# Performance work log

Measured on AMD Instinct MI355X. Metric: run time of the kernel, lower is better.

## Reference

```python
import jax, jax.numpy as jnp
import numpy as np

N = 100000
D = 128      # embedding_dim
HID = 32     # hidden per head
HEADS = 4
OUT_C = 64
E = 1600000
NEG_SLOPE = 0.2


def setup_inputs() -> dict:
    key = jax.random.key(0)
    ks = jax.random.split(key, 12)
    inp = {}
    inp["x_indices"] = jnp.arange(N, dtype=jnp.int64)
    inp["ei"] = jax.random.randint(ks[0], (2, E), 0, N, dtype=jnp.int64)
    # parameters
    inp["emb"] = jax.random.normal(ks[1], (N, D), dtype=jnp.float32)
    # conv1: in=D, out=HID per head, HEADS heads, concat
    s1 = 1.0 / np.sqrt(D)
    inp["W1"] = jax.random.normal(ks[2], (D, HEADS * HID), dtype=jnp.float32) * s1
    inp["a_src1"] = jax.random.normal(ks[3], (HEADS, HID), dtype=jnp.float32) * s1
    inp["a_dst1"] = jax.random.normal(ks[4], (HEADS, HID), dtype=jnp.float32) * s1
    inp["b1"] = jnp.zeros((HEADS * HID,), dtype=jnp.float32)
    # conv2: in=HEADS*HID, out=OUT_C, 1 head
    s2 = 1.0 / np.sqrt(HEADS * HID)
    inp["W2"] = jax.random.normal(ks[5], (HEADS * HID, OUT_C), dtype=jnp.float32) * s2
    inp["a_src2"] = jax.random.normal(ks[6], (1, OUT_C), dtype=jnp.float32) * s2
    inp["a_dst2"] = jax.random.normal(ks[7], (1, OUT_C), dtype=jnp.float32) * s2
    inp["b2"] = jnp.zeros((OUT_C,), dtype=jnp.float32)
    return inp


def gat_conv(x, src, dst, W, a_src, a_dst, b, heads, out_ch, concat):
    # x: [N, Din]; src/dst: [E'] (self-loops already included)
    n = x.shape[0]
    h = (x @ W).reshape(n, heads, out_ch)          # [N, H, C]
    alpha_s = jnp.sum(h * a_src, axis=-1)          # [N, H]
    alpha_d = jnp.sum(h * a_dst, axis=-1)          # [N, H]
    e = alpha_s[src] + alpha_d[dst]                # [E', H]
    e = jnp.where(e > 0, e, NEG_SLOPE * e)         # leaky_relu
    # segment softmax over incoming edges per destination node
    m = jax.ops.segment_max(e, dst, num_segments=n)      # [N, H]
    ex = jnp.exp(e - m[dst])
    den = jax.ops.segment_sum(ex, dst, num_segments=n)   # [N, H]
    a = ex / den[dst]                              # [E', H]  (self-loops guarantee den>0)
    msg = h[src] * a[:, :, None]                   # [E', H, C]
    out = jax.ops.segment_sum(msg, dst, num_segments=n)  # [N, H, C]
    if concat:
        out = out.reshape(n, heads * out_ch)
    else:
        out = out.mean(axis=1)
    return out + b


def reference(x_indices, ei, emb, W1, a_src1, a_dst1, b1, W2, a_src2, a_dst2, b2):
    n = emb.shape[0]
    # PyG GATConv default add_self_loops=True
    loop = jnp.arange(n, dtype=ei.dtype)
    src = jnp.concatenate([ei[0], loop])
    dst = jnp.concatenate([ei[1], loop])
    x = emb[x_indices]                                  # embedding lookup
    x = jax.nn.elu(gat_conv(x, src, dst, W1, a_src1, a_dst1, b1, HEADS, HID, True))
    # dropout p=0.5 is identity in eval mode
    return gat_conv(x, src, dst, W2, a_src2, a_dst2, b2, 1, OUT_C, True)
```

## Files before the change

kernel.cpp:

```cpp
#include <hip/hip_runtime.h>
#include <math.h>

#define NEG_SLOPE 0.2f
#define BK_SHIFT 8

typedef __attribute__((ext_vector_type(2))) float v2f;
typedef __attribute__((ext_vector_type(8))) short bf16x8;
typedef __attribute__((ext_vector_type(4))) float f32x4;

__device__ __forceinline__ float leaky(float x) { return x > 0.f ? x : NEG_SLOPE * x; }
__device__ __forceinline__ float dot4(float4 a, float4 b) {
    return a.x * b.x + a.y * b.y + a.z * b.z + a.w * b.w;
}
__device__ __forceinline__ unsigned short f2bf(float f) {
    unsigned int x = __float_as_uint(f);
    unsigned int r = (x + 0x7fffu + ((x >> 16) & 1u)) >> 16;
    return (unsigned short)r;
}
__device__ __forceinline__ float bflo(unsigned int u) { return __uint_as_float(u << 16); }
__device__ __forceinline__ float bfhi(unsigned int u) { return __uint_as_float(u & 0xffff0000u); }


__global__ void __launch_bounds__(256) bcount_kernel(const int* __restrict__ ei, int E, int E2,
                                                     int K, int* __restrict__ bcounts) {
    __shared__ int h[512];
    int t = threadIdx.x;
    h[t] = 0; h[t + 256] = 0;
    __syncthreads();
    int base = blockIdx.x * 4096;
#pragma unroll 4
    for (int i = 0; i < 16; i++) {
        int e = base + i * 256 + t;
        if (e < E2) {
            int dst = (e < E) ? ei[E + e] : (e - E);
            atomicAdd(&h[dst >> BK_SHIFT], 1);
        }
    }
    __syncthreads();
    for (int b = t; b < K; b += 256) {
        int c = h[b];
        if (c) atomicAdd(&bcounts[b], c);
    }
}

__global__ void __launch_bounds__(512) bscan_kernel(const int* __restrict__ bcounts, int K,
                                                    int* __restrict__ bbase, int* __restrict__ bcursor) {
    __shared__ int s[512];
    int t = threadIdx.x;
    int v = (t < K) ? bcounts[t] : 0;
    s[t] = v;
    __syncthreads();
    for (int off = 1; off < 512; off <<= 1) {
        int u = (t >= off) ? s[t - off] : 0;
        __syncthreads();
        s[t] += u;
        __syncthreads();
    }
    if (t < K) {
        int ex = s[t] - v;
        bbase[t] = ex;
        bcursor[t] = ex;
    }
    if (t == 511) bbase[K] = s[511];
}

__global__ void __launch_bounds__(256) bscatter_kernel(const int* __restrict__ ei, int E, int E2,
                                                       int K, int* __restrict__ bcursor,
                                                       unsigned int* __restrict__ bedges) {
    __shared__ int hist[512], pre[512], lcur[512], gbase[512], psum[256];
    __shared__ unsigned int stage[4096];
    __shared__ unsigned short binof[4096];
    int t = threadIdx.x;
    hist[t] = 0; hist[t + 256] = 0;
    __syncthreads();
    int base = blockIdx.x * 4096;
    int cnt = min(4096, E2 - base);
    int s_[16], d_[16];
#pragma unroll
    for (int i = 0; i < 16; i++) {
        int e = base + i * 256 + t;
        if (e < E2) {
            int ss, dd;
            if (e < E) { ss = ei[e]; dd = ei[E + e]; }
            else       { ss = e - E; dd = ss; }
            s_[i] = ss; d_[i] = dd;
            atomicAdd(&hist[dd >> BK_SHIFT], 1);
        }
    }
    __syncthreads();
    int a0 = hist[2 * t], a1 = hist[2 * t + 1];
    psum[t] = a0 + a1;
    __syncthreads();
    for (int off = 1; off < 256; off <<= 1) {
        int u = (t >= off) ? psum[t - off] : 0;
        __syncthreads();
        psum[t] += u;
        __syncthreads();
    }
    int pex = psum[t] - (a0 + a1);
    pre[2 * t] = pex;
    pre[2 * t + 1] = pex + a0;
    __syncthreads();
    for (int b = t; b < K; b += 256) {
        int c = hist[b];
        if (c) gbase[b] = atomicAdd(&bcursor[b], c);
    }
    lcur[t] = pre[t]; lcur[t + 256] = pre[t + 256];
    __syncthreads();
#pragma unroll
    for (int i = 0; i < 16; i++) {
        int e = base + i * 256 + t;
        if (e < E2) {
            int bin = d_[i] >> BK_SHIFT;
            int p = atomicAdd(&lcur[bin], 1);
            stage[p] = ((unsigned)s_[i] << 8) | (unsigned)(d_[i] & 255);
            binof[p] = (unsigned short)bin;
        }
    }
    __syncthreads();
    for (int i = t; i < cnt; i += 256) {
        unsigned int ed = stage[i];
        int bin = (int)binof[i];
        bedges[gbase[bin] + (i - pre[bin])] = ed;
    }
}

__global__ void __launch_bounds__(256) bcsr_kernel(const unsigned int* __restrict__ bedges,
                                                   const int* __restrict__ bbase, int N,
                                                   int* __restrict__ counts, int* __restrict__ indptr,
                                                   int* __restrict__ csr) {
    __shared__ int hist[256], scn[256], cur[256];
    int b = blockIdx.x;
    int t = threadIdx.x;
    int base = bbase[b];
    int cnt = bbase[b + 1] - base;
    hist[t] = 0;
    __syncthreads();
    for (int i = t; i < cnt; i += 256) {
        atomicAdd(&hist[bedges[base + i] & 255u], 1);
    }
    __syncthreads();
    int v = hist[t];
    scn[t] = v;
    __syncthreads();
    for (int off = 1; off < 256; off <<= 1) {
        int u = (t >= off) ? scn[t - off] : 0;
        __syncthreads();
        scn[t] += u;
        __syncthreads();
    }
    int ex = scn[t] - v;
    int d = (b << BK_SHIFT) + t;
    if (d < N) { counts[d] = v; indptr[d] = base + ex; }
    cur[t] = ex;
    __syncthreads();
    for (int i = t; i < cnt; i += 256) {
        unsigned int ed = bedges[base + i];
        int p = atomicAdd(&cur[ed & 255u], 1);
        csr[base + p] = (int)(ed >> 8);
    }
}


__global__ void w2pack_kernel(const float* __restrict__ W2, unsigned short* __restrict__ w2p) {
    int i = blockIdx.x * 256 + threadIdx.x;
    if (i < 8192) {
        int t = i >> 11;
        int c = (i >> 9) & 3;
        int l = (i >> 3) & 63;
        int j = i & 7;
        int k = t * 32 + (l >> 4) * 8 + j;
        int col = c * 16 + (l & 15);
        w2p[i] = f2bf(W2[k * 64 + col]);
    }
}


__device__ __forceinline__ void fma16(float4 xv, float4 wv0, float4 wv1,
                                      float4 wv2, float4 wv3, float4& a) {
    a.x = fmaf(xv.x, wv0.x, a.x); a.y = fmaf(xv.x, wv0.y, a.y);
    a.z = fmaf(xv.x, wv0.z, a.z); a.w = fmaf(xv.x, wv0.w, a.w);
    a.x = fmaf(xv.y, wv1.x, a.x); a.y = fmaf(xv.y, wv1.y, a.y);
    a.z = fmaf(xv.y, wv1.z, a.z); a.w = fmaf(xv.y, wv1.w, a.w);
    a.x = fmaf(xv.z, wv2.x, a.x); a.y = fmaf(xv.z, wv2.y, a.y);
    a.z = fmaf(xv.z, wv2.z, a.z); a.w = fmaf(xv.z, wv2.w, a.w);
    a.x = fmaf(xv.w, wv3.x, a.x); a.y = fmaf(xv.w, wv3.y, a.y);
    a.z = fmaf(xv.w, wv3.z, a.z); a.w = fmaf(xv.w, wv3.w, a.w);
}


__global__ __launch_bounds__(256) void gemm1_kernel(const float* __restrict__ emb,
                             const int* __restrict__ xidx,
                             const float* __restrict__ W1,
                             unsigned short* __restrict__ h1b,
                             const float* __restrict__ a_s1, const float* __restrict__ a_d1,
                             float* __restrict__ as1, float* __restrict__ ad1, int N) {
    __shared__ float xs[64][64];
    __shared__ float ws[64][128];
    int tid = threadIdx.x;
    int r0 = blockIdx.x * 64;
    int tr = tid >> 5;
    int tc = tid & 31;
    float4 acc[8];
#pragma unroll
    for (int i = 0; i < 8; i++) acc[i] = make_float4(0.f, 0.f, 0.f, 0.f);
    const float4* W4 = (const float4*)W1;
    const float4* emb4 = (const float4*)emb;
    float4* ws4 = (float4*)ws;
    float4* xs4 = (float4*)xs;

    for (int half = 0; half < 2; half++) {
        float4 wbuf[8];
#pragma unroll
        for (int j = 0; j < 8; j++) wbuf[j] = W4[half * 2048 + tid + j * 256];
        float4 xbuf[4];
#pragma unroll
        for (int j = 0; j < 4; j++) {
            int idx = tid + j * 256;
            int r = idx >> 4, c = idx & 15;
            int row = r0 + r;
            float4 v = make_float4(0.f, 0.f, 0.f, 0.f);
            if (row < N) {
                int s = xidx[row];
                v = emb4[(size_t)s * 32 + half * 16 + c];
            }
            xbuf[j] = v;
        }
        __syncthreads();
#pragma unroll
        for (int j = 0; j < 8; j++) ws4[tid + j * 256] = wbuf[j];
#pragma unroll
        for (int j = 0; j < 4; j++) xs4[tid + j * 256] = xbuf[j];
        __syncthreads();
        for (int k = 0; k < 64; k += 4) {
            float4 wv0 = *(const float4*)&ws[k][tc * 4];
            float4 wv1 = *(const float4*)&ws[k + 1][tc * 4];
            float4 wv2 = *(const float4*)&ws[k + 2][tc * 4];
            float4 wv3 = *(const float4*)&ws[k + 3][tc * 4];
#pragma unroll
            for (int i = 0; i < 8; i++) {
                float4 xv = *(const float4*)&xs[tr * 8 + i][k];
                fma16(xv, wv0, wv1, wv2, wv3, acc[i]);
            }
        }
    }
    int colbase = tc * 4;
    int h = tc >> 3;
    int off = (tc & 7) * 4;
    float4 av = *(const float4*)&a_s1[h * 32 + off];
    float4 dv = *(const float4*)&a_d1[h * 32 + off];
#pragma unroll
    for (int i = 0; i < 8; i++) {
        int row = r0 + tr * 8 + i;
        if (row < N) {
            ushort4 pk;
            pk.x = f2bf(acc[i].x); pk.y = f2bf(acc[i].y);
            pk.z = f2bf(acc[i].z); pk.w = f2bf(acc[i].w);
            *(ushort4*)&h1b[(size_t)row * 128 + colbase] = pk;
        }
        float ps = dot4(acc[i], av);
        float pd = dot4(acc[i], dv);
        ps += __shfl_xor(ps, 1); pd += __shfl_xor(pd, 1);
        ps += __shfl_xor(ps, 2); pd += __shfl_xor(pd, 2);
        ps += __shfl_xor(ps, 4); pd += __shfl_xor(pd, 4);
        if ((tc & 7) == 0 && row < N) {
            as1[row * 4 + h] = ps;
            ad1[row * 4 + h] = pd;
        }
    }
}


__device__ __forceinline__ void edge_fma(uint4 u0, float w, v2f* acc) {
    v2f wv = {w, w};
    v2f t;
    t.x = bflo(u0.x); t.y = bfhi(u0.x); acc[0] += wv * t;
    t.x = bflo(u0.y); t.y = bfhi(u0.y); acc[1] += wv * t;
    t.x = bflo(u0.z); t.y = bfhi(u0.z); acc[2] += wv * t;
    t.x = bflo(u0.w); t.y = bfhi(u0.w); acc[3] += wv * t;
}

__device__ __forceinline__ void accum_tbl1(int srcReg, const float* __restrict__ ew, int mcount,
                                           const uint4* __restrict__ h1v4,
                                           int lanebase, int sub, int cg, int hh, v2f* acc) {
    int b = 0;
    for (; b + 8 <= mcount; b += 8) {
        int i0 = b + sub, i1 = b + 2 + sub, i2 = b + 4 + sub, i3 = b + 6 + sub;
        int s0 = __shfl(srcReg, lanebase + i0);
        int s1 = __shfl(srcReg, lanebase + i1);
        int s2 = __shfl(srcReg, lanebase + i2);
        int s3 = __shfl(srcReg, lanebase + i3);
        float w_0 = ew[i0 * 4 + hh];
        float w_1 = ew[i1 * 4 + hh];
        float w_2 = ew[i2 * 4 + hh];
        float w_3 = ew[i3 * 4 + hh];
        uint4 u0 = h1v4[(unsigned)(s0 * 16 + cg)];
        uint4 u1 = h1v4[(unsigned)(s1 * 16 + cg)];
        uint4 u2 = h1v4[(unsigned)(s2 * 16 + cg)];
        uint4 u3 = h1v4[(unsigned)(s3 * 16 + cg)];
        edge_fma(u0, w_0, acc);
        edge_fma(u1, w_1, acc);
        edge_fma(u2, w_2, acc);
        edge_fma(u3, w_3, acc);
    }
    if (b + 4 <= mcount) {
        int i0 = b + sub, i1 = b + 2 + sub;
        int s0 = __shfl(srcReg, lanebase + i0);
        int s1 = __shfl(srcReg, lanebase + i1);
        float w_0 = ew[i0 * 4 + hh];
        float w_1 = ew[i1 * 4 + hh];
        uint4 u0 = h1v4[(unsigned)(s0 * 16 + cg)];
        uint4 u1 = h1v4[(unsigned)(s1 * 16 + cg)];
        edge_fma(u0, w_0, acc);
        edge_fma(u1, w_1, acc);
        b += 4;
    }
    if (b + 2 <= mcount) {
        int i0 = b + sub;
        int s0 = __shfl(srcReg, lanebase + i0);
        float w_0 = ew[i0 * 4 + hh];
        uint4 u0 = h1v4[(unsigned)(s0 * 16 + cg)];
        edge_fma(u0, w_0, acc);
        b += 2;
    }
    if (b < mcount) {
        int s0 = __shfl(srcReg, lanebase + b);
        if (sub == 0) {
            float w_0 = ew[b * 4 + hh];
            uint4 u0 = h1v4[(unsigned)(s0 * 16 + cg)];
            edge_fma(u0, w_0, acc);
        }
    }
}

__global__ void __launch_bounds__(256)
agg1_kernel(const int* __restrict__ csr, const int* __restrict__ indptr,
            const int* __restrict__ counts, const float* __restrict__ as1,
            const float* __restrict__ ad1, const unsigned short* __restrict__ h1b,
            const float* __restrict__ b1, const unsigned short* __restrict__ w2p,
            const float* __restrict__ a_s2, const float* __restrict__ a_d2,
            unsigned short* __restrict__ h2b, float* __restrict__ as2,
            float* __restrict__ ad2, int N) {
    __shared__ __attribute__((aligned(16))) float ewt[4][2][128];
    __shared__ __attribute__((aligned(16))) unsigned short w2s[8192];
    int tid = threadIdx.x;
    {
        const uint4* w4 = (const uint4*)w2p;
        uint4* s4 = (uint4*)w2s;
        for (int i = tid; i < 1024; i += 256) s4[i] = w4[i];
    }
    __syncthreads();

    int lane = tid & 63;
    int wv = tid >> 6;
    int l32 = lane & 31;
    int lanebase = lane & 32;
    int n = blockIdx.x * 8 + wv * 2 + (lane >> 5);
    bool valid = (n < N);
    int nsafe = valid ? n : 0;
    int start = indptr[nsafe];
    int cnt = valid ? counts[nsafe] : 0;
    float4 ad4 = ((const float4*)ad1)[nsafe];

    int src0 = 0;
    float4 p0 = make_float4(0.f, 0.f, 0.f, 0.f);
    if (l32 < cnt) {
        src0 = csr[start + l32];
        float4 a = ((const float4*)as1)[src0];
        p0.x = __expf(leaky(a.x + ad4.x));
        p0.y = __expf(leaky(a.y + ad4.y));
        p0.z = __expf(leaky(a.z + ad4.z));
        p0.w = __expf(leaky(a.w + ad4.w));
    }
    float4 l4 = p0;
    if (cnt > 32) {
        for (int base = 32; base < cnt; base += 32) {
            if (base + l32 < cnt) {
                int s = csr[start + base + l32];
                float4 a = ((const float4*)as1)[s];
                l4.x += __expf(leaky(a.x + ad4.x));
                l4.y += __expf(leaky(a.y + ad4.y));
                l4.z += __expf(leaky(a.z + ad4.z));
                l4.w += __expf(leaky(a.w + ad4.w));
            }
        }
    }
#pragma unroll
    for (int off = 16; off >= 1; off >>= 1) {
        l4.x += __shfl_xor(l4.x, off);
        l4.y += __shfl_xor(l4.y, off);
        l4.z += __shfl_xor(l4.z, off);
        l4.w += __shfl_xor(l4.w, off);
    }
    float4 li = make_float4(1.f / l4.x, 1.f / l4.y, 1.f / l4.z, 1.f / l4.w);
    float4 w0 = make_float4(p0.x * li.x, p0.y * li.y, p0.z * li.z, p0.w * li.w);

    float* ew = ewt[wv][lane >> 5];
    *(float4*)&ew[l32 * 4] = w0;

    int sub = l32 >> 4;
    int cg = lane & 15;
    int hh = cg >> 2;
    const uint4* h1v4 = (const uint4*)h1b;
    v2f acc[4];
    acc[0] = acc[1] = acc[2] = acc[3] = (v2f){0.f, 0.f};
    accum_tbl1(src0, ew, min(cnt, 32), h1v4, lanebase, sub, cg, hh, acc);
    if (cnt > 32) {
        for (int base = 32; base < cnt; base += 32) {
            int srcc = 0;
            float4 wc = make_float4(0.f, 0.f, 0.f, 0.f);
            if (base + l32 < cnt) {
                srcc = csr[start + base + l32];
                float4 a = ((const float4*)as1)[srcc];
                wc.x = __expf(leaky(a.x + ad4.x)) * li.x;
                wc.y = __expf(leaky(a.y + ad4.y)) * li.y;
                wc.z = __expf(leaky(a.z + ad4.z)) * li.z;
                wc.w = __expf(leaky(a.w + ad4.w)) * li.w;
            }
            *(float4*)&ew[l32 * 4] = wc;
            accum_tbl1(srcc, ew, min(cnt - base, 32), h1v4, lanebase, sub, cg, hh, acc);
        }
    }
#pragma unroll
    for (int i = 0; i < 4; i++) {
        acc[i].x += __shfl_xor(acc[i].x, 16);
        acc[i].y += __shfl_xor(acc[i].y, 16);
    }
    unsigned short* xa = (unsigned short*)&ewt[wv][0][0];
    if (l32 < 16) {
        const float4* b4 = (const float4*)b1;
        float4 ba = b4[cg * 2], bb = b4[cg * 2 + 1];
        float o[8];
        o[0] = acc[0].x + ba.x; o[1] = acc[0].y + ba.y;
        o[2] = acc[1].x + ba.z; o[3] = acc[1].y + ba.w;
        o[4] = acc[2].x + bb.x; o[5] = acc[2].y + bb.y;
        o[6] = acc[3].x + bb.z; o[7] = acc[3].y + bb.w;
#pragma unroll
        for (int j = 0; j < 8; j++) o[j] = (o[j] > 0.f) ? o[j] : (__expf(o[j]) - 1.f);
        uint4 pk;
        pk.x = (unsigned)f2bf(o[0]) | ((unsigned)f2bf(o[1]) << 16);
        pk.y = (unsigned)f2bf(o[2]) | ((unsigned)f2bf(o[3]) << 16);
        pk.z = (unsigned)f2bf(o[4]) | ((unsigned)f2bf(o[5]) << 16);
        pk.w = (unsigned)f2bf(o[6]) | ((unsigned)f2bf(o[7]) << 16);
        *(uint4*)&xa[cg * 16 + (lane >> 5) * 8] = pk;
    }
    int rowA = lane & 15;
    int kb = lane >> 4;
    f32x4 hacc[4];
#pragma unroll
    for (int c = 0; c < 4; c++) hacc[c] = (f32x4){0.f, 0.f, 0.f, 0.f};
#pragma unroll
    for (int t = 0; t < 4; t++) {
        bf16x8 af = {0, 0, 0, 0, 0, 0, 0, 0};
        if (rowA < 2) af = *(const bf16x8*)&xa[(t * 4 + kb) * 16 + rowA * 8];
#pragma unroll
        for (int c = 0; c < 4; c++) {
            bf16x8 bf = *(const bf16x8*)&w2s[((t * 4 + c) * 64 + lane) * 8];
            hacc[c] = __builtin_amdgcn_mfma_f32_16x16x32_bf16(af, bf, hacc[c], 0, 0, 0);
        }
    }
    int na = blockIdx.x * 8 + wv * 2;
    int nb = na + 1;
    bool va = (na < N), vb = (nb < N);
    if (lane < 16) {
        float psa = 0.f, pda = 0.f, psb = 0.f, pdb = 0.f;
#pragma unroll
        for (int c = 0; c < 4; c++) {
            float h0 = hacc[c][0];
            float h1r = hacc[c][1];
            float asv = a_s2[c * 16 + lane];
            float adv = a_d2[c * 16 + lane];
            psa = fmaf(h0, asv, psa); pda = fmaf(h0, adv, pda);
            psb = fmaf(h1r, asv, psb); pdb = fmaf(h1r, adv, pdb);
            if (va) h2b[(size_t)na * 64 + c * 16 + lane] = f2bf(h0);
            if (vb) h2b[(size_t)nb * 64 + c * 16 + lane] = f2bf(h1r);
        }
#pragma unroll
        for (int off = 8; off >= 1; off >>= 1) {
            psa += __shfl_xor(psa, off); pda += __shfl_xor(pda, off);
            psb += __shfl_xor(psb, off); pdb += __shfl_xor(pdb, off);
        }
        if (lane == 0) {
            if (va) { as2[na] = psa; ad2[na] = pda; }
            if (vb) { as2[nb] = psb; ad2[nb] = pdb; }
        }
    }
}


__device__ __forceinline__ void accum2(int srcReg, float wReg, int mcount,
                                       const uint4* __restrict__ h2v4,
                                       int lanebase, int sub, int cg, v2f* acc) {
    int b = 0;
    for (; b + 16 <= mcount; b += 16) {
        int i0 = b + sub, i1 = b + 4 + sub, i2 = b + 8 + sub, i3 = b + 12 + sub;
        int s0 = __shfl(srcReg, lanebase + i0);
        int s1 = __shfl(srcReg, lanebase + i1);
        int s2 = __shfl(srcReg, lanebase + i2);
        int s3 = __shfl(srcReg, lanebase + i3);
        float w_0 = __shfl(wReg, lanebase + i0);
        float w_1 = __shfl(wReg, lanebase + i1);
        float w_2 = __shfl(wReg, lanebase + i2);
        float w_3 = __shfl(wReg, lanebase + i3);
        uint4 u0 = h2v4[(unsigned)(s0 * 8 + cg)];
        uint4 u1 = h2v4[(unsigned)(s1 * 8 + cg)];
        uint4 u2 = h2v4[(unsigned)(s2 * 8 + cg)];
        uint4 u3 = h2v4[(unsigned)(s3 * 8 + cg)];
        edge_fma(u0, w_0, acc);
        edge_fma(u1, w_1, acc);
        edge_fma(u2, w_2, acc);
        edge_fma(u3, w_3, acc);
    }
    if (b + 8 <= mcount) {
        int i0 = b + sub, i1 = b + 4 + sub;
        int s0 = __shfl(srcReg, lanebase + i0);
        int s1 = __shfl(srcReg, lanebase + i1);
        float w_0 = __shfl(wReg, lanebase + i0);
        float w_1 = __shfl(wReg, lanebase + i1);
        uint4 u0 = h2v4[(unsigned)(s0 * 8 + cg)];
        uint4 u1 = h2v4[(unsigned)(s1 * 8 + cg)];
        edge_fma(u0, w_0, acc);
        edge_fma(u1, w_1, acc);
        b += 8;
    }
    if (b + 4 <= mcount) {
        int i0 = b + sub;
        int s0 = __shfl(srcReg, lanebase + i0);
        float w_0 = __shfl(wReg, lanebase + i0);
        uint4 u0 = h2v4[(unsigned)(s0 * 8 + cg)];
        edge_fma(u0, w_0, acc);
        b += 4;
    }
    if (b < mcount) {
        int rem = mcount - b;
        int i0 = b + sub;
        int ic = min(i0, mcount - 1);
        int s0 = __shfl(srcReg, lanebase + ic);
        float w_0 = __shfl(wReg, lanebase + ic);
        if (sub < rem) {
            uint4 u0 = h2v4[(unsigned)(s0 * 8 + cg)];
            edge_fma(u0, w_0, acc);
        }
    }
}

__global__ void __launch_bounds__(256)
agg2_kernel(const int* __restrict__ csr, const int* __restrict__ indptr,
            const int* __restrict__ counts, const float* __restrict__ as2,
            const float* __restrict__ ad2, const unsigned short* __restrict__ h2b,
            const float* __restrict__ b2, float* __restrict__ out, int N) {
    int lane = threadIdx.x & 63;
    int l32 = lane & 31;
    int lanebase = lane & 32;
    int n = blockIdx.x * 8 + (threadIdx.x >> 6) * 2 + (lane >> 5);
    if (n >= N) return;
    int start = indptr[n];
    int cnt = counts[n];
    float ad = ad2[n];

    int src0 = 0;
    float p0 = 0.f;
    if (l32 < cnt) {
        src0 = csr[start + l32];
        p0 = __expf(leaky(as2[src0] + ad));
    }
    float l = p0;
    if (cnt > 32) {
        for (int base = 32; base < cnt; base += 32) {
            if (base + l32 < cnt)
                l += __expf(leaky(as2[csr[start + base + l32]] + ad));
        }
    }
#pragma unroll
    for (int off = 16; off >= 1; off >>= 1) l += __shfl_xor(l, off);
    float li = 1.f / l;
    float w0 = p0 * li;

    int sub = l32 >> 3;
    int cg = lane & 7;
    const uint4* h2v4 = (const uint4*)h2b;
    v2f acc[4];
    acc[0] = acc[1] = acc[2] = acc[3] = (v2f){0.f, 0.f};
    accum2(src0, w0, min(cnt, 32), h2v4, lanebase, sub, cg, acc);
    if (cnt > 32) {
        for (int base = 32; base < cnt; base += 32) {
            int srcc = 0;
            float wc = 0.f;
            if (base + l32 < cnt) {
                srcc = csr[start + base + l32];
                wc = __expf(leaky(as2[srcc] + ad)) * li;
            }
            accum2(srcc, wc, min(cnt - base, 32), h2v4, lanebase, sub, cg, acc);
        }
    }
#pragma unroll
    for (int i = 0; i < 4; i++) {
        acc[i].x += __shfl_xor(acc[i].x, 8);
        acc[i].x += __shfl_xor(acc[i].x, 16);
        acc[i].y += __shfl_xor(acc[i].y, 8);
        acc[i].y += __shfl_xor(acc[i].y, 16);
    }
    if (l32 < 8) {
        const float4* b4 = (const float4*)b2;
        float4 ba = b4[cg * 2], bb = b4[cg * 2 + 1];
        float4 o0, o1;
        o0.x = acc[0].x + ba.x; o0.y = acc[0].y + ba.y;
        o0.z = acc[1].x + ba.z; o0.w = acc[1].y + ba.w;
        o1.x = acc[2].x + bb.x; o1.y = acc[2].y + bb.y;
        o1.z = acc[3].x + bb.z; o1.w = acc[3].y + bb.w;
        float4* orow = (float4*)&out[(size_t)n * 64 + cg * 8];
        orow[0] = o0;
        orow[1] = o1;
    }
}


extern "C" void kernel_launch(void* const* d_in, const int* in_sizes, int n_in,
                              void* d_out, int out_size, void* d_ws, size_t ws_size,
                              hipStream_t stream) {
    const int*   xidx = (const int*)d_in[0];
    const int*   ei   = (const int*)d_in[1];
    const float* emb  = (const float*)d_in[2];
    const float* W1   = (const float*)d_in[3];
    const float* a_s1 = (const float*)d_in[4];
    const float* a_d1 = (const float*)d_in[5];
    const float* b1   = (const float*)d_in[6];
    const float* W2   = (const float*)d_in[7];
    const float* a_s2 = (const float*)d_in[8];
    const float* a_d2 = (const float*)d_in[9];
    const float* b2   = (const float*)d_in[10];
    float* out = (float*)d_out;

    const int N  = in_sizes[0];
    const int E  = in_sizes[1] / 2;
    const int E2 = E + N;
    const int K  = (N + 255) >> BK_SHIFT;

    int* ws_i    = (int*)d_ws;
    int* counts  = ws_i;
    int* indptr  = ws_i + N;
    int* bcounts = ws_i + 2 * (size_t)N;
    int* bbase   = ws_i + 2 * (size_t)N + 512;
    int* bcursor = ws_i + 2 * (size_t)N + 1032;
    int* csr     = ws_i + 2 * (size_t)N + 1544;
    size_t fbase = ((size_t)(2 * (size_t)N + 1544 + E2) + 3) & ~(size_t)3;
    float* ws_f = (float*)d_ws;
    unsigned short* h1b = (unsigned short*)(ws_f + fbase);
    float* region2 = ws_f + fbase + (size_t)N * 64;
    unsigned short* h2b = (unsigned short*)region2;
    float* as2 = region2 + (size_t)N * 32;
    float* ad2 = region2 + (size_t)N * 33;
    unsigned short* w2p = (unsigned short*)(region2 + (size_t)N * 34);
    float* as1 = ws_f + fbase + (size_t)N * 128;
    float* ad1 = as1 + (size_t)N * 4;
    unsigned int* bedges = (unsigned int*)region2;

    int nchunks = (E2 + 4095) / 4096;
    hipMemsetAsync(bcounts, 0, (size_t)K * sizeof(int), stream);
    bcount_kernel<<<nchunks, 256, 0, stream>>>(ei, E, E2, K, bcounts);
    bscan_kernel<<<1, 512, 0, stream>>>(bcounts, K, bbase, bcursor);
    bscatter_kernel<<<nchunks, 256, 0, stream>>>(ei, E, E2, K, bcursor, bedges);
    bcsr_kernel<<<K, 256, 0, stream>>>(bedges, bbase, N, counts, indptr, csr);

    gemm1_kernel<<<(N + 63) / 64, 256, 0, stream>>>(emb, xidx, W1, h1b, a_s1, a_d1, as1, ad1, N);

    w2pack_kernel<<<32, 256, 0, stream>>>(W2, w2p);

    agg1_kernel<<<(N + 7) / 8, 256, 0, stream>>>(csr, indptr, counts, as1, ad1, h1b, b1,
                                                 w2p, a_s2, a_d2, h2b, as2, ad2, N);

    agg2_kernel<<<(N + 7) / 8, 256, 0, stream>>>(csr, indptr, counts, as2, ad2, h2b, b2, out, N);
}
```

Baseline: 401.3 us.

## Move first-layer GEMM to split-bf16 MFMA and merge prep kernels

Replaces the FP32 scalar-FMA tiled GEMM for layer 1 with bf16 MFMA 16x16x32 instructions. A hi/lo split (three MFMAs per tile) keeps accuracy close to FP32. A new prep kernel packs W1 into hi/lo bf16 fragments, packs W2, and zeroes the bucket counters, replacing the memset and the separate w2pack launch. This removes a launch and shifts the GEMM onto matrix cores, but triples the MFMA work and adds bf16 conversion cost per element. The attention-score reduction now uses 16-lane shuffles.

```diff
diff --git a/kernel.cpp b/kernel.cpp
--- a/kernel.cpp
+++ b/kernel.cpp
@@ -9,9 +9,6 @@
 typedef __attribute__((ext_vector_type(4))) float f32x4;
 
 __device__ __forceinline__ float leaky(float x) { return x > 0.f ? x : NEG_SLOPE * x; }
-__device__ __forceinline__ float dot4(float4 a, float4 b) {
-    return a.x * b.x + a.y * b.y + a.z * b.z + a.w * b.w;
-}
 __device__ __forceinline__ unsigned short f2bf(float f) {
     unsigned int x = __float_as_uint(f);
     unsigned int r = (x + 0x7fffu + ((x >> 16) & 1u)) >> 16;
@@ -19,6 +16,33 @@
 }
 __device__ __forceinline__ float bflo(unsigned int u) { return __uint_as_float(u << 16); }
 __device__ __forceinline__ float bfhi(unsigned int u) { return __uint_as_float(u & 0xffff0000u); }
+
+
+__global__ void __launch_bounds__(256) prep_kernel(const float* __restrict__ W1,
+                                                   const float* __restrict__ W2,
+                                                   unsigned short* __restrict__ w1ph,
+                                                   unsigned short* __restrict__ w1pl,
+                                                   unsigned short* __restrict__ w2p,
+                                                   int* __restrict__ bcounts) {
+    int i = blockIdx.x * 256 + threadIdx.x;
+    if (i < 16384) {
+        int j = i & 7, l = (i >> 3) & 63, c = (i >> 9) & 7, t = i >> 12;
+        int k = t * 32 + ((l >> 4) << 3) + j;
+        int col = c * 16 + (l & 15);
+        float v = W1[k * 128 + col];
+        unsigned short hi = f2bf(v);
+        w1ph[i] = hi;
+        w1pl[i] = f2bf(v - __uint_as_float((unsigned)hi << 16));
+    } else if (i < 16384 + 8192) {
+        int i2 = i - 16384;
+        int t = i2 >> 11, c = (i2 >> 9) & 3, l = (i2 >> 3) & 63, j = i2 & 7;
+        int k = t * 32 + (l >> 4) * 8 + j;
+        int col = c * 16 + (l & 15);
+        w2p[i2] = f2bf(W2[k * 64 + col]);
+    } else if (i < 16384 + 8192 + 512) {
+        bcounts[i - 16384 - 8192] = 0;
+    }
+}
 
 
 __global__ void __launch_bounds__(256) bcount_kernel(const int* __restrict__ ei, int E, int E2,
@@ -162,110 +186,103 @@
 }
 
 
-__global__ void w2pack_kernel(const float* __restrict__ W2, unsigned short* __restrict__ w2p) {
-    int i = blockIdx.x * 256 + threadIdx.x;
-    if (i < 8192) {
-        int t = i >> 11;
-        int c = (i >> 9) & 3;
-        int l = (i >> 3) & 63;
-        int j = i & 7;
-        int k = t * 32 + (l >> 4) * 8 + j;
-        int col = c * 16 + (l & 15);
-        w2p[i] = f2bf(W2[k * 64 + col]);
-    }
-}
-
-
-__device__ __forceinline__ void fma16(float4 xv, float4 wv0, float4 wv1,
-                                      float4 wv2, float4 wv3, float4& a) {
-    a.x = fmaf(xv.x, wv0.x, a.x); a.y = fmaf(xv.x, wv0.y, a.y);
-    a.z = fmaf(xv.x, wv0.z, a.z); a.w = fmaf(xv.x, wv0.w, a.w);
-    a.x = fmaf(xv.y, wv1.x, a.x); a.y = fmaf(xv.y, wv1.y, a.y);
-    a.z = fmaf(xv.y, wv1.z, a.z); a.w = fmaf(xv.y, wv1.w, a.w);
-    a.x = fmaf(xv.z, wv2.x, a.x); a.y = fmaf(xv.z, wv2.y, a.y);
-    a.z = fmaf(xv.z, wv2.z, a.z); a.w = fmaf(xv.z, wv2.w, a.w);
-    a.x = fmaf(xv.w, wv3.x, a.x); a.y = fmaf(xv.w, wv3.y, a.y);
-    a.z = fmaf(xv.w, wv3.z, a.z); a.w = fmaf(xv.w, wv3.w, a.w);
-}
-
-
 __global__ __launch_bounds__(256) void gemm1_kernel(const float* __restrict__ emb,
                              const int* __restrict__ xidx,
-                             const float* __restrict__ W1,
+                             const unsigned short* __restrict__ w1ph,
+                             const unsigned short* __restrict__ w1pl,
                              unsigned short* __restrict__ h1b,
                              const float* __restrict__ a_s1, const float* __restrict__ a_d1,
                              float* __restrict__ as1, float* __restrict__ ad1, int N) {
-    __shared__ float xs[64][64];
-    __shared__ float ws[64][128];
+    __shared__ __attribute__((aligned(16))) unsigned short w1s[2][16384];
     int tid = threadIdx.x;
-    int r0 = blockIdx.x * 64;
-    int tr = tid >> 5;
-    int tc = tid & 31;
-    float4 acc[8];
-#pragma unroll
-    for (int i = 0; i < 8; i++) acc[i] = make_float4(0.f, 0.f, 0.f, 0.f);
-    const float4* W4 = (const float4*)W1;
-    const float4* emb4 = (const float4*)emb;
-    float4* ws4 = (float4*)ws;
-    float4* xs4 = (float4*)xs;
-
-    for (int half = 0; half < 2; half++) {
-        float4 wbuf[8];
-#pragma unroll
-        for (int j = 0; j < 8; j++) wbuf[j] = W4[half * 2048 + tid + j * 256];
-        float4 xbuf[4];
-#pragma unroll
-        for (int j = 0; j < 4; j++) {
-            int idx = tid + j * 256;
-            int r = idx >> 4, c = idx & 15;
-            int row = r0 + r;
-            float4 v = make_float4(0.f, 0.f, 0.f, 0.f);
-            if (row < N) {
-                int s = xidx[row];
-                v = emb4[(size_t)s * 32 + half * 16 + c];
-            }
-            xbuf[j] = v;
-        }
-        __syncthreads();
-#pragma unroll
-        for (int j = 0; j < 8; j++) ws4[tid + j * 256] = wbuf[j];
-#pragma unroll
-        for (int j = 0; j < 4; j++) xs4[tid + j * 256] = xbuf[j];
-        __syncthreads();
-        for (int k = 0; k < 64; k += 4) {
-            float4 wv0 = *(const float4*)&ws[k][tc * 4];
-            float4 wv1 = *(const float4*)&ws[k + 1][tc * 4];
-            float4 wv2 = *(const float4*)&ws[k + 2][tc * 4];
-            float4 wv3 = *(const float4*)&ws[k + 3][tc * 4];
-#pragma unroll
-            for (int i = 0; i < 8; i++) {
-                float4 xv = *(const float4*)&xs[tr * 8 + i][k];
-                fma16(xv, wv0, wv1, wv2, wv3, acc[i]);
-            }
-        }
-    }
-    int colbase = tc * 4;
-    int h = tc >> 3;
-    int off = (tc & 7) * 4;
-    float4 av = *(const float4*)&a_s1[h * 32 + off];
-    float4 dv = *(const float4*)&a_d1[h * 32 + off];
-#pragma unroll
-    for (int i = 0; i < 8; i++) {
-        int row = r0 + tr * 8 + i;
-        if (row < N) {
-            ushort4 pk;
-            pk.x = f2bf(acc[i].x); pk.y = f2bf(acc[i].y);
-            pk.z = f2bf(acc[i].z); pk.w = f2bf(acc[i].w);
-            *(ushort4*)&h1b[(size_t)row * 128 + colbase] = pk;
-        }
-        float ps = dot4(acc[i], av);
-        float pd = dot4(acc[i], dv);
-        ps += __shfl_xor(ps, 1); pd += __shfl_xor(pd, 1);
-        ps += __shfl_xor(ps, 2); pd += __shfl_xor(pd, 2);
-        ps += __shfl_xor(ps, 4); pd += __shfl_xor(pd, 4);
-        if ((tc & 7) == 0 && row < N) {
-            as1[row * 4 + h] = ps;
-            ad1[row * 4 + h] = pd;
+    {
+        const uint4* h4 = (const uint4*)w1ph;
+        const uint4* l4 = (const uint4*)w1pl;
+        uint4* sh = (uint4*)w1s[0];
+        uint4* sl = (uint4*)w1s[1];
+        for (int i = tid; i < 2048; i += 256) { sh[i] = h4[i]; sl[i] = l4[i]; }
+    }
+    __syncthreads();
+    int lane = tid & 63;
+    int wv = tid >> 6;
+    int l15 = lane & 15;
+    int kb = lane >> 4;
+    int r0 = blockIdx.x * 128 + wv * 32;
+    int sA[2];
+#pragma unroll
+    for (int rt = 0; rt < 2; rt++) {
+        int r = r0 + rt * 16 + l15;
+        sA[rt] = xidx[min(r, N - 1)];
+    }
+    f32x4 acc[2][8];
+#pragma unroll
+    for (int rt = 0; rt < 2; rt++)
+#pragma unroll
+        for (int c = 0; c < 8; c++) acc[rt][c] = (f32x4){0.f, 0.f, 0.f, 0.f};
+
+#pragma unroll
+    for (int t = 0; t < 4; t++) {
+        bf16x8 ahi[2], alo[2];
+#pragma unroll
+        for (int rt = 0; rt < 2; rt++) {
+            const float* ap = emb + (size_t)sA[rt] * 128 + t * 32 + kb * 8;
+            float4 a0 = *(const float4*)ap;
+            float4 a1 = *(const float4*)(ap + 4);
+            float av[8] = {a0.x, a0.y, a0.z, a0.w, a1.x, a1.y, a1.z, a1.w};
+#pragma unroll
+            for (int j = 0; j < 8; j++) {
+                unsigned short hi = f2bf(av[j]);
+                ahi[rt][j] = (short)hi;
+                alo[rt][j] = (short)f2bf(av[j] - __uint_as_float((unsigned)hi << 16));
+            }
+        }
+#pragma unroll
+        for (int c = 0; c < 8; c++) {
+            bf16x8 bhi = *(const bf16x8*)&w1s[0][((t * 8 + c) * 64 + lane) * 8];
+            bf16x8 blo = *(const bf16x8*)&w1s[1][((t * 8 + c) * 64 + lane) * 8];
+#pragma unroll
+            for (int rt = 0; rt < 2; rt++) {
+                acc[rt][c] = __builtin_amdgcn_mfma_f32_16x16x32_bf16(ahi[rt], bhi, acc[rt][c], 0, 0, 0);
+                acc[rt][c] = __builtin_amdgcn_mfma_f32_16x16x32_bf16(alo[rt], bhi, acc[rt][c], 0, 0, 0);
+                acc[rt][c] = __builtin_amdgcn_mfma_f32_16x16x32_bf16(ahi[rt], blo, acc[rt][c], 0, 0, 0);
+            }
+        }
+    }
+    float asv[8], adv[8];
+#pragma unroll
+    for (int c = 0; c < 8; c++) {
+        asv[c] = a_s1[c * 16 + l15];
+        adv[c] = a_d1[c * 16 + l15];
+    }
+#pragma unroll
+    for (int rt = 0; rt < 2; rt++) {
+#pragma unroll
+        for (int reg = 0; reg < 4; reg++) {
+            int row = r0 + rt * 16 + kb * 4 + reg;
+            bool vr = row < N;
+            if (vr) {
+#pragma unroll
+                for (int c = 0; c < 8; c++)
+                    h1b[(size_t)row * 128 + c * 16 + l15] = f2bf(acc[rt][c][reg]);
+            }
+            float ps[4], pd[4];
+#pragma unroll
+            for (int h = 0; h < 4; h++) {
+                ps[h] = acc[rt][2 * h][reg] * asv[2 * h] + acc[rt][2 * h + 1][reg] * asv[2 * h + 1];
+                pd[h] = acc[rt][2 * h][reg] * adv[2 * h] + acc[rt][2 * h + 1][reg] * adv[2 * h + 1];
+            }
+#pragma unroll
+            for (int off = 1; off <= 8; off <<= 1) {
+#pragma unroll
+                for (int h = 0; h < 4; h++) {
+                    ps[h] += __shfl_xor(ps[h], off);
+                    pd[h] += __shfl_xor(pd[h], off);
+                }
+            }
+            if (l15 == 0 && vr) {
+                *(float4*)&as1[row * 4] = make_float4(ps[0], ps[1], ps[2], ps[3]);
+                *(float4*)&ad1[row * 4] = make_float4(pd[0], pd[1], pd[2], pd[3]);
+            }
         }
     }
 }
@@ -650,21 +667,23 @@
     unsigned short* h2b = (unsigned short*)region2;
     float* as2 = region2 + (size_t)N * 32;
     float* ad2 = region2 + (size_t)N * 33;
-    unsigned short* w2p = (unsigned short*)(region2 + (size_t)N * 34);
+    unsigned short* w2p  = (unsigned short*)(region2 + (size_t)N * 34);
+    unsigned short* w1ph = (unsigned short*)(region2 + (size_t)N * 34 + 4096);
+    unsigned short* w1pl = (unsigned short*)(region2 + (size_t)N * 34 + 12288);
     float* as1 = ws_f + fbase + (size_t)N * 128;
     float* ad1 = as1 + (size_t)N * 4;
     unsigned int* bedges = (unsigned int*)region2;
 
+    prep_kernel<<<(16384 + 8192 + 512 + 255) / 256, 256, 0, stream>>>(W1, W2, w1ph, w1pl, w2p, bcounts);
+
     int nchunks = (E2 + 4095) / 4096;
-    hipMemsetAsync(bcounts, 0, (size_t)K * sizeof(int), stream);
     bcount_kernel<<<nchunks, 256, 0, stream>>>(ei, E, E2, K, bcounts);
     bscan_kernel<<<1, 512, 0, stream>>>(bcounts, K, bbase, bcursor);
     bscatter_kernel<<<nchunks, 256, 0, stream>>>(ei, E, E2, K, bcursor, bedges);
     bcsr_kernel<<<K, 256, 0, stream>>>(bedges, bbase, N, counts, indptr, csr);
 
-    gemm1_kernel<<<(N + 63) / 64, 256, 0, stream>>>(emb, xidx, W1, h1b, a_s1, a_d1, as1, ad1, N);
-
-    w2pack_kernel<<<32, 256, 0, stream>>>(W2, w2p);
+    gemm1_kernel<<<(N + 127) / 128, 256, 0, stream>>>(emb, xidx, w1ph, w1pl, h1b,
+                                                      a_s1, a_d1, as1, ad1, N);
 
     agg1_kernel<<<(N + 7) / 8, 256, 0, stream>>>(csr, indptr, counts, as1, ad1, h1b, b1,
                                                  w2p, a_s2, a_d2, h2b, as2, ad2, N);
```

After: 354.1 us. 11.8% less time.
